# Kernel tuning notes

Measured on AMD Instinct MI355X. Metric: run time of the kernel, lower is better.

The kernel has to match this reference:

```python
import jax, jax.numpy as jnp
import numpy as np

K0 = 16                       # probe slice length (hard-coded in kernel)
TAU = 2.053748910631823       # t-test threshold (|tau| of kernel constant)


def setup_inputs() -> dict:
    key = jax.random.key(0)
    k1, k2, k3 = jax.random.split(key, 3)
    B, DIN, DOUT = 8192, 4096, 4096
    x = jax.random.normal(k1, (B, DIN), dtype=jnp.float32)
    W = jax.random.normal(k2, (DOUT, DIN), dtype=jnp.float32)
    bias = jax.random.normal(k3, (DOUT,), dtype=jnp.float32)
    return {"x": x, "W": W, "bias": bias}


def reference(x, W, bias):
    # --- partial dot over the first K0 columns of K (the probe) ---
    x0 = x[:, :K0]                    # [B, K0]
    w0 = W[:, :K0]                    # [DOUT, K0]
    y1 = x0 @ w0.T                    # [B, DOUT]  sum_k x_k * w_k
    # sum of squared elementwise products: prod_k^2 = x_k^2 * w_k^2
    s2 = (x0 * x0) @ (w0 * w0).T      # [B, DOUT]
    # --- per-(row, column) t-statistic and early-exit decision ---
    tstat = jnp.abs(y1) / jnp.sqrt(s2 / K0)
    passed = tstat < TAU              # True -> column deemed insignificant, zeroed
    # --- full linear (active columns keep full accumulation + bias) ---
    full = x @ W.T + bias[None, :]    # [B, DOUT]
    return jnp.where(passed, 0.0, full)
```

## Files before the change

kernel.cpp:

```cpp
#include <hip/hip_runtime.h>
#include <cstdint>
#include <cstddef>

#define TAU_D 2.053748910631823
#define M_DIM 8192
#define N_DIM 4096
#define K_DIM 4096
#define NT64  (K_DIM / 64)

typedef float f32x4 __attribute__((ext_vector_type(4)));
typedef short bf16x8 __attribute__((ext_vector_type(8)));

typedef __attribute__((address_space(1))) void gvoid_t;
typedef __attribute__((address_space(3))) void lvoid_t;

__device__ __forceinline__ void gload_lds16(const void* g, void* l) {
    __builtin_amdgcn_global_load_lds((const gvoid_t*)g, (lvoid_t*)l, 16, 0, 0);
}

__device__ __forceinline__ unsigned int pack2bf(float lo, float hi) {
    unsigned int ul = __float_as_uint(lo);
    unsigned int uh = __float_as_uint(hi);
    ul = (ul + 0x7FFFu + ((ul >> 16) & 1u)) >> 16;
    uh = (uh + 0x7FFFu + ((uh >> 16) & 1u)) >> 16;
    return ul | (uh << 16);
}

__global__ void cvt_f32_to_bf16(const float4* __restrict__ in,
                                uint2* __restrict__ out, int n4) {
    int i = blockIdx.x * blockDim.x + threadIdx.x;
    const int stride = gridDim.x * blockDim.x;
    for (; i < n4; i += stride) {
        float4 a = in[i];
        uint2 o;
        o.x = pack2bf(a.x, a.y);
        o.y = pack2bf(a.z, a.w);
        out[i] = o;
    }
}

__global__ __launch_bounds__(512, 2) void gemm_masked8(
    const unsigned short* __restrict__ Ab,
    const unsigned short* __restrict__ Bb,
    const float* __restrict__ X,
    const float* __restrict__ Wt,
    const float* __restrict__ bias,
    float* __restrict__ out)
{
    __shared__ __align__(16) char lds[131072];

    const int tid  = threadIdx.x;
    const int wave = tid >> 6;
    const int lane = tid & 63;
    const int lr = lane & 15;
    const int lq = lane >> 4;
    const int wm = wave >> 2;
    const int wn = wave & 3;

    const int flat = blockIdx.x;
    const int xcd  = flat & 7;
    const int s    = flat >> 3;
    const int rnd  = s >> 5;
    const int jj   = s & 31;
    const int trow = rnd * 16 + ((xcd >> 2) << 3) + (jj >> 2);
    const int tcol = ((xcd & 3) << 2) + (jj & 3);
    const int rowBase = trow * 256;
    const int colBase = tcol * 256;

    f32x4 acc[8][4];
    #pragma unroll
    for (int i = 0; i < 8; ++i)
        #pragma unroll
        for (int n = 0; n < 4; ++n)
            acc[i][n] = (f32x4){0.f, 0.f, 0.f, 0.f};

    const int srow  = tid >> 3;
    const int sslot = (tid & 7) ^ (srow & 7);
    const unsigned short* aSrc =
        Ab + (size_t)(rowBase + srow) * K_DIM + sslot * 8;
    const unsigned short* bSrc =
        Bb + (size_t)(colBase + srow) * K_DIM + sslot * 8;

    const unsigned baseA = (unsigned)(wm * 128 + lr) * 128;
    const unsigned baseB = 32768u + (unsigned)(wn * 64 + lr) * 128;
    const unsigned sk0 = (unsigned)((lq) ^ (lr & 7)) * 16;
    const unsigned sk1 = (unsigned)((4 + lq) ^ (lr & 7)) * 16;

    #pragma unroll
    for (int i = 0; i < 4; ++i)
        gload_lds16(aSrc + (size_t)i * 64 * K_DIM,
                    lds + i * 8192 + wave * 1024);
    #pragma unroll
    for (int i = 0; i < 4; ++i)
        gload_lds16(bSrc + (size_t)i * 64 * K_DIM,
                    lds + 32768 + i * 8192 + wave * 1024);
    __syncthreads();

    for (int T = 0; T < NT64; ++T) {
        const bool st = (T + 1 < NT64);
        const unsigned cb = (unsigned)(T & 1) << 16;
        const unsigned ob = cb ^ 65536u;
        const char* L = lds + cb;
        const unsigned short* aS = aSrc + (size_t)(T + 1) * 64;
        const unsigned short* bS = bSrc + (size_t)(T + 1) * 64;

        bf16x8 af[4], bq[4];

        #pragma unroll
        for (int m = 0; m < 4; ++m)
            af[m] = *(const bf16x8*)(L + baseA + m * 2048 + sk0);
        #pragma unroll
        for (int n = 0; n < 4; ++n)
            bq[n] = *(const bf16x8*)(L + baseB + n * 2048 + sk0);
        if (st) {
            #pragma unroll
            for (int i = 0; i < 4; ++i)
                gload_lds16(aS + (size_t)i * 64 * K_DIM,
                            lds + ob + i * 8192 + wave * 1024);
        }
        __builtin_amdgcn_s_barrier();
        __builtin_amdgcn_sched_barrier(0);
        __builtin_amdgcn_s_setprio(1);
        #pragma unroll
        for (int m = 0; m < 4; ++m)
            #pragma unroll
            for (int n = 0; n < 4; ++n)
                acc[m][n] = __builtin_amdgcn_mfma_f32_16x16x32_bf16(
                    af[m], bq[n], acc[m][n], 0, 0, 0);
        __builtin_amdgcn_s_setprio(0);
        __builtin_amdgcn_s_barrier();
        __builtin_amdgcn_sched_barrier(0);

        #pragma unroll
        for (int m = 0; m < 4; ++m)
            af[m] = *(const bf16x8*)(L + baseA + (4 + m) * 2048 + sk0);
        if (st) {
            #pragma unroll
            for (int i = 0; i < 4; ++i)
                gload_lds16(bS + (size_t)i * 64 * K_DIM,
                            lds + ob + 32768 + i * 8192 + wave * 1024);
        }
        __builtin_amdgcn_s_barrier();
        __builtin_amdgcn_sched_barrier(0);
        __builtin_amdgcn_s_setprio(1);
        #pragma unroll
        for (int m = 0; m < 4; ++m)
            #pragma unroll
            for (int n = 0; n < 4; ++n)
                acc[4 + m][n] = __builtin_amdgcn_mfma_f32_16x16x32_bf16(
                    af[m], bq[n], acc[4 + m][n], 0, 0, 0);
        __builtin_amdgcn_s_setprio(0);
        __builtin_amdgcn_s_barrier();
        __builtin_amdgcn_sched_barrier(0);

        #pragma unroll
        for (int m = 0; m < 4; ++m)
            af[m] = *(const bf16x8*)(L + baseA + m * 2048 + sk1);
        #pragma unroll
        for (int n = 0; n < 4; ++n)
            bq[n] = *(const bf16x8*)(L + baseB + n * 2048 + sk1);
        __builtin_amdgcn_s_barrier();
        __builtin_amdgcn_sched_barrier(0);
        __builtin_amdgcn_s_setprio(1);
        #pragma unroll
        for (int m = 0; m < 4; ++m)
            #pragma unroll
            for (int n = 0; n < 4; ++n)
                acc[m][n] = __builtin_amdgcn_mfma_f32_16x16x32_bf16(
                    af[m], bq[n], acc[m][n], 0, 0, 0);
        __builtin_amdgcn_s_setprio(0);
        __builtin_amdgcn_s_barrier();
        __builtin_amdgcn_sched_barrier(0);

        #pragma unroll
        for (int m = 0; m < 4; ++m)
            af[m] = *(const bf16x8*)(L + baseA + (4 + m) * 2048 + sk1);
        __builtin_amdgcn_s_barrier();
        __builtin_amdgcn_sched_barrier(0);
        __builtin_amdgcn_s_setprio(1);
        #pragma unroll
        for (int m = 0; m < 4; ++m)
            #pragma unroll
            for (int n = 0; n < 4; ++n)
                acc[4 + m][n] = __builtin_amdgcn_mfma_f32_16x16x32_bf16(
                    af[m], bq[n], acc[4 + m][n], 0, 0, 0);
        __builtin_amdgcn_s_setprio(0);

        __syncthreads();
    }

    float* x0s = (float*)(lds);
    float* w0s = (float*)(lds + 16384);
    #pragma unroll
    for (int i = 0; i < 2; ++i) {
        int idx = tid + i * 512;
        int r = idx >> 2, qq = (idx & 3) << 2;
        *(f32x4*)(x0s + r * 16 + qq) =
            *(const f32x4*)(X + (size_t)(rowBase + r) * K_DIM + qq);
        *(f32x4*)(w0s + r * 16 + qq) =
            *(const f32x4*)(Wt + (size_t)(colBase + r) * K_DIM + qq);
    }
    __syncthreads();

    const float TAU32 = (float)TAU_D;

    #pragma unroll
    for (int np = 0; np < 4; np += 2) {
        float wv[2][16];
        float bv[2];
        #pragma unroll
        for (int e = 0; e < 2; ++e) {
            const int c = wn * 64 + (np + e) * 16 + lr;
            #pragma unroll
            for (int q = 0; q < 4; ++q)
                *(f32x4*)&wv[e][q * 4] = *(const f32x4*)(w0s + c * 16 + q * 4);
            bv[e] = bias[colBase + c];
        }
        #pragma unroll
        for (int mi = 0; mi < 8; ++mi) {
            #pragma unroll
            for (int j = 0; j < 4; ++j) {
                const int rw = wm * 128 + mi * 16 + lq * 4 + j;
                float xv[16];
                #pragma unroll
                for (int q = 0; q < 4; ++q)
                    *(f32x4*)&xv[q * 4] = *(const f32x4*)(x0s + rw * 16 + q * 4);
                const size_t orow = (size_t)(rowBase + rw) * N_DIM + colBase;
                #pragma unroll
                for (int e = 0; e < 2; ++e) {
                    const int n = np + e;
                    float y1 = 0.f, s2 = 0.f;
                    #pragma unroll
                    for (int k = 0; k < 16; ++k) {
                        float xk = xv[k], wk = wv[e][k];
                        float xx = xk * xk, ww = wk * wk;
                        y1 = fmaf(xk, wk, y1);
                        s2 = fmaf(xx, ww, s2);
                    }
                    float t = fabsf(y1) / sqrtf(s2 * 0.0625f);
                    float v = (t < TAU32) ? 0.0f : (acc[mi][n][j] + bv[e]);
                    out[orow + wn * 64 + n * 16 + lr] = v;
                }
            }
        }
    }
}

__global__ __launch_bounds__(256, 2) void gemm_masked_fb(
    const float* __restrict__ X, const float* __restrict__ Wt,
    const float* __restrict__ bias, float* __restrict__ out)
{
    __shared__ __align__(16) unsigned short As[128 * 32];
    __shared__ __align__(16) unsigned short Bs[128 * 32];

    const int tid  = threadIdx.x;
    const int wave = tid >> 6;
    const int lane = tid & 63;
    const int rowBase = blockIdx.y * 128;
    const int colBase = blockIdx.x * 128;
    const int wr = wave >> 1;
    const int wc = wave & 1;
    const int lr = lane & 15;
    const int lq = lane >> 4;

    f32x4 acc[4][4];
    #pragma unroll
    for (int m = 0; m < 4; ++m)
        #pragma unroll
        for (int n = 0; n < 4; ++n)
            acc[m][n] = (f32x4){0.f, 0.f, 0.f, 0.f};

    const int srow = tid >> 2;
    const int scol = (tid & 3) * 8;
    const float* afp = X  + (size_t)(rowBase + srow) * K_DIM + scol;
    const float* bfp = Wt + (size_t)(colBase + srow) * K_DIM + scol;

    for (int kt = 0; kt < K_DIM; kt += 32) {
        #pragma unroll
        for (int issue = 0; issue < 2; ++issue) {
            const float* sa = afp + (size_t)issue * 64 * K_DIM;
            const float* sb = bfp + (size_t)issue * 64 * K_DIM;
            float4 a0 = *(const float4*)(sa);
            float4 a1 = *(const float4*)(sa + 4);
            float4 b0 = *(const float4*)(sb);
            float4 b1 = *(const float4*)(sb + 4);
            uint4 pa, pb;
            pa.x = pack2bf(a0.x, a0.y); pa.y = pack2bf(a0.z, a0.w);
            pa.z = pack2bf(a1.x, a1.y); pa.w = pack2bf(a1.z, a1.w);
            pb.x = pack2bf(b0.x, b0.y); pb.y = pack2bf(b0.z, b0.w);
            pb.z = pack2bf(b1.x, b1.y); pb.w = pack2bf(b1.z, b1.w);
            *(uint4*)((char*)As + issue * 4096 + tid * 16) = pa;
            *(uint4*)((char*)Bs + issue * 4096 + tid * 16) = pb;
        }
        afp += 32; bfp += 32;
        __syncthreads();

        bf16x8 af[4], bq[4];
        #pragma unroll
        for (int m = 0; m < 4; ++m)
            af[m] = *(const bf16x8*)(As + (wr * 64 + m * 16 + lr) * 32 + lq * 8);
        #pragma unroll
        for (int n = 0; n < 4; ++n)
            bq[n] = *(const bf16x8*)(Bs + (wc * 64 + n * 16 + lr) * 32 + lq * 8);
        #pragma unroll
        for (int m = 0; m < 4; ++m)
            #pragma unroll
            for (int n = 0; n < 4; ++n)
                acc[m][n] = __builtin_amdgcn_mfma_f32_16x16x32_bf16(
                    af[m], bq[n], acc[m][n], 0, 0, 0);
        __syncthreads();
    }

    float* x0s = (float*)As;
    float* w0s = (float*)Bs;
    #pragma unroll
    for (int i = 0; i < 2; ++i) {
        int idx = tid + i * 256;
        int r = idx >> 2, q = (idx & 3) * 4;
        *(float4*)(x0s + r * 16 + q) =
            *(const float4*)(X + (size_t)(rowBase + r) * K_DIM + q);
        *(float4*)(w0s + r * 16 + q) =
            *(const float4*)(Wt + (size_t)(colBase + r) * K_DIM + q);
    }
    __syncthreads();

    const float TAU32 = (float)TAU_D;
    float wv[4][16];
    float bv[4];
    #pragma unroll
    for (int n = 0; n < 4; ++n) {
        int c = wc * 64 + n * 16 + lr;
        #pragma unroll
        for (int q = 0; q < 4; ++q)
            *(f32x4*)&wv[n][q * 4] = *(const f32x4*)(w0s + c * 16 + q * 4);
        bv[n] = bias[colBase + c];
    }

    #pragma unroll
    for (int m = 0; m < 4; ++m) {
        #pragma unroll
        for (int j = 0; j < 4; ++j) {
            const int r = wr * 64 + m * 16 + lq * 4 + j;
            float xv[16];
            #pragma unroll
            for (int q = 0; q < 4; ++q)
                *(f32x4*)&xv[q * 4] = *(const f32x4*)(x0s + r * 16 + q * 4);
            const size_t orow = (size_t)(rowBase + r) * N_DIM + colBase;
            #pragma unroll
            for (int n = 0; n < 4; ++n) {
                float y1 = 0.f, s2 = 0.f;
                #pragma unroll
                for (int k = 0; k < 16; ++k) {
                    float xk = xv[k];
                    float wk = wv[n][k];
                    float xx = xk * xk;
                    float ww = wk * wk;
                    y1 = fmaf(xk, wk, y1);
                    s2 = fmaf(xx, ww, s2);
                }
                float t = fabsf(y1) / sqrtf(s2 * 0.0625f);
                float v = (t < TAU32) ? 0.0f : (acc[m][n][j] + bv[n]);
                out[orow + wc * 64 + n * 16 + lr] = v;
            }
        }
    }
}

extern "C" void kernel_launch(void* const* d_in, const int* in_sizes, int n_in,
                              void* d_out, int out_size, void* d_ws, size_t ws_size,
                              hipStream_t stream) {
    const float* x    = (const float*)d_in[0];
    const float* W    = (const float*)d_in[1];
    const float* bias = (const float*)d_in[2];
    float* out = (float*)d_out;

    const size_t needA = (size_t)M_DIM * K_DIM * 2;
    const size_t needB = (size_t)N_DIM * K_DIM * 2;

    if (ws_size >= needA + needB) {
        unsigned short* xb = (unsigned short*)d_ws;
        unsigned short* wb = (unsigned short*)((char*)d_ws + needA);
        cvt_f32_to_bf16<<<2048, 256, 0, stream>>>(
            (const float4*)x, (uint2*)xb, (M_DIM * K_DIM) / 4);
        cvt_f32_to_bf16<<<2048, 256, 0, stream>>>(
            (const float4*)W, (uint2*)wb, (N_DIM * K_DIM) / 4);
        dim3 grid((M_DIM / 256) * (N_DIM / 256));
        gemm_masked8<<<grid, 512, 0, stream>>>(xb, wb, x, W, bias, out);
    } else {
        dim3 grid(N_DIM / 128, M_DIM / 128);
        gemm_masked_fb<<<grid, 256, 0, stream>>>(x, W, bias, out);
    }
}
```

Baseline: 331.2 us.

## Switch GEMM main loop to triple-buffered K=32 stages with vmcnt-based waits

Measured after the change: 353.1 us. 1.07x slower.

```diff
diff --git a/kernel.cpp b/kernel.cpp
--- a/kernel.cpp
+++ b/kernel.cpp
@@ -6,7 +6,7 @@
 #define M_DIM 8192
 #define N_DIM 4096
 #define K_DIM 4096
-#define NT64  (K_DIM / 64)
+#define NT32  (K_DIM / 32)
 
 typedef float f32x4 __attribute__((ext_vector_type(4)));
 typedef short bf16x8 __attribute__((ext_vector_type(8)));
@@ -47,7 +47,7 @@
     const float* __restrict__ bias,
     float* __restrict__ out)
 {
-    __shared__ __align__(16) char lds[131072];
+    __shared__ __align__(16) char lds[98304];
 
     const int tid  = threadIdx.x;
     const int wave = tid >> 6;
@@ -74,49 +74,54 @@
         for (int n = 0; n < 4; ++n)
             acc[i][n] = (f32x4){0.f, 0.f, 0.f, 0.f};
 
-    const int srow  = tid >> 3;
-    const int sslot = (tid & 7) ^ (srow & 7);
+    const int srow = tid >> 2;
+    const int slog = ((tid & 3) - ((tid >> 3) & 3)) & 3;
     const unsigned short* aSrc =
-        Ab + (size_t)(rowBase + srow) * K_DIM + sslot * 8;
+        Ab + (size_t)(rowBase + srow) * K_DIM + slog * 8;
     const unsigned short* bSrc =
-        Bb + (size_t)(colBase + srow) * K_DIM + sslot * 8;
-
-    const unsigned baseA = (unsigned)(wm * 128 + lr) * 128;
-    const unsigned baseB = 32768u + (unsigned)(wn * 64 + lr) * 128;
-    const unsigned sk0 = (unsigned)((lq) ^ (lr & 7)) * 16;
-    const unsigned sk1 = (unsigned)((4 + lq) ^ (lr & 7)) * 16;
-
-    #pragma unroll
-    for (int i = 0; i < 4; ++i)
-        gload_lds16(aSrc + (size_t)i * 64 * K_DIM,
-                    lds + i * 8192 + wave * 1024);
-    #pragma unroll
-    for (int i = 0; i < 4; ++i)
-        gload_lds16(bSrc + (size_t)i * 64 * K_DIM,
-                    lds + 32768 + i * 8192 + wave * 1024);
-    __syncthreads();
-
-    for (int T = 0; T < NT64; ++T) {
-        const bool st = (T + 1 < NT64);
-        const unsigned cb = (unsigned)(T & 1) << 16;
-        const unsigned ob = cb ^ 65536u;
-        const char* L = lds + cb;
-        const unsigned short* aS = aSrc + (size_t)(T + 1) * 64;
-        const unsigned short* bS = bSrc + (size_t)(T + 1) * 64;
+        Bb + (size_t)(colBase + srow) * K_DIM + slog * 8;
+
+    const unsigned skrot = (unsigned)((lq + (lr >> 1)) & 3) * 16;
+    const unsigned offA0 = (unsigned)(wm * 128 + lr) * 64 + skrot;
+    const unsigned offB0 = 16384u + (unsigned)(wn * 64 + lr) * 64 + skrot;
+
+    unsigned b0 = 0, b1 = 32768, b2 = 65536;
+
+    #pragma unroll
+    for (int i = 0; i < 2; ++i)
+        gload_lds16(aSrc + (size_t)i * 128 * K_DIM, lds + b0 + i * 8192 + wave * 1024);
+    #pragma unroll
+    for (int i = 0; i < 2; ++i)
+        gload_lds16(bSrc + (size_t)i * 128 * K_DIM, lds + b0 + 16384 + i * 8192 + wave * 1024);
+    #pragma unroll
+    for (int i = 0; i < 2; ++i)
+        gload_lds16(aSrc + 32 + (size_t)i * 128 * K_DIM, lds + b1 + i * 8192 + wave * 1024);
+    #pragma unroll
+    for (int i = 0; i < 2; ++i)
+        gload_lds16(bSrc + 32 + (size_t)i * 128 * K_DIM, lds + b1 + 16384 + i * 8192 + wave * 1024);
+    asm volatile("s_waitcnt vmcnt(4)" ::: "memory");
+    __builtin_amdgcn_s_barrier();
+    __builtin_amdgcn_sched_barrier(0);
+
+    for (int T = 0; T < NT32; ++T) {
+        const bool st = (T + 2 < NT32);
+        const char* L = lds + b0;
+        const unsigned short* aS = aSrc + (size_t)(T + 2) * 32;
+        const unsigned short* bS = bSrc + (size_t)(T + 2) * 32;
 
         bf16x8 af[4], bq[4];
 
         #pragma unroll
         for (int m = 0; m < 4; ++m)
-            af[m] = *(const bf16x8*)(L + baseA + m * 2048 + sk0);
+            af[m] = *(const bf16x8*)(L + offA0 + m * 1024);
         #pragma unroll
         for (int n = 0; n < 4; ++n)
-            bq[n] = *(const bf16x8*)(L + baseB + n * 2048 + sk0);
+            bq[n] = *(const bf16x8*)(L + offB0 + n * 1024);
         if (st) {
             #pragma unroll
-            for (int i = 0; i < 4; ++i)
-                gload_lds16(aS + (size_t)i * 64 * K_DIM,
-                            lds + ob + i * 8192 + wave * 1024);
+            for (int i = 0; i < 2; ++i)
+                gload_lds16(aS + (size_t)i * 128 * K_DIM,
+                            lds + b2 + i * 8192 + wave * 1024);
         }
         __builtin_amdgcn_s_barrier();
         __builtin_amdgcn_sched_barrier(0);
@@ -133,12 +138,12 @@
 
         #pragma unroll
         for (int m = 0; m < 4; ++m)
-            af[m] = *(const bf16x8*)(L + baseA + (4 + m) * 2048 + sk0);
+            af[m] = *(const bf16x8*)(L + offA0 + (4 + m) * 1024);
         if (st) {
             #pragma unroll
-            for (int i = 0; i < 4; ++i)
-                gload_lds16(bS + (size_t)i * 64 * K_DIM,
-                            lds + ob + 32768 + i * 8192 + wave * 1024);
+            for (int i = 0; i < 2; ++i)
+                gload_lds16(bS + (size_t)i * 128 * K_DIM,
+                            lds + b2 + 16384 + i * 8192 + wave * 1024);
         }
         __builtin_amdgcn_s_barrier();
         __builtin_amdgcn_sched_barrier(0);
@@ -150,43 +155,16 @@
                 acc[4 + m][n] = __builtin_amdgcn_mfma_f32_16x16x32_bf16(
                     af[m], bq[n], acc[4 + m][n], 0, 0, 0);
         __builtin_amdgcn_s_setprio(0);
+
+        if (T < NT32 - 2) {
+            asm volatile("s_waitcnt vmcnt(4)" ::: "memory");
+        } else if (T == NT32 - 2) {
+            asm volatile("s_waitcnt vmcnt(0)" ::: "memory");
+        }
         __builtin_amdgcn_s_barrier();
         __builtin_amdgcn_sched_barrier(0);
 
-        #pragma unroll
-        for (int m = 0; m < 4; ++m)
-            af[m] = *(const bf16x8*)(L + baseA + m * 2048 + sk1);
-        #pragma unroll
-        for (int n = 0; n < 4; ++n)
-            bq[n] = *(const bf16x8*)(L + baseB + n * 2048 + sk1);
-        __builtin_amdgcn_s_barrier();
-        __builtin_amdgcn_sched_barrier(0);
-        __builtin_amdgcn_s_setprio(1);
-        #pragma unroll
-        for (int m = 0; m < 4; ++m)
-            #pragma unroll
-            for (int n = 0; n < 4; ++n)
-                acc[m][n] = __builtin_amdgcn_mfma_f32_16x16x32_bf16(
-                    af[m], bq[n], acc[m][n], 0, 0, 0);
-        __builtin_amdgcn_s_setprio(0);
-        __builtin_amdgcn_s_barrier();
-        __builtin_amdgcn_sched_barrier(0);
-
-        #pragma unroll
-        for (int m = 0; m < 4; ++m)
-            af[m] = *(const bf16x8*)(L + baseA + (4 + m) * 2048 + sk1);
-        __builtin_amdgcn_s_barrier();
-        __builtin_amdgcn_sched_barrier(0);
-        __builtin_amdgcn_s_setprio(1);
-        #pragma unroll
-        for (int m = 0; m < 4; ++m)
-            #pragma unroll
-            for (int n = 0; n < 4; ++n)
-                acc[4 + m][n] = __builtin_amdgcn_mfma_f32_16x16x32_bf16(
-                    af[m], bq[n], acc[4 + m][n], 0, 0, 0);
-        __builtin_amdgcn_s_setprio(0);
-
-        __syncthreads();
+        unsigned t = b0; b0 = b1; b1 = b2; b2 = t;
     }
 
     float* x0s = (float*)(lds);
```

## Restructure GEMM main loop into an 8-phase pipeline with split A/B LDS staging

Applied to the files above, without the earlier changes.

Measured after the change: 325.0 us. About the same (-1.9%).

```diff
diff --git a/kernel.cpp b/kernel.cpp
--- a/kernel.cpp
+++ b/kernel.cpp
@@ -6,9 +6,9 @@
 #define M_DIM 8192
 #define N_DIM 4096
 #define K_DIM 4096
-#define NT64  (K_DIM / 64)
-
-typedef float f32x4 __attribute__((ext_vector_type(4)));
+#define NIT   32
+
+typedef float f32x4  __attribute__((ext_vector_type(4)));
 typedef short bf16x8 __attribute__((ext_vector_type(8)));
 
 typedef __attribute__((address_space(1))) void gvoid_t;
@@ -39,6 +39,9 @@
     }
 }
 
+#define BARRIER() do { __builtin_amdgcn_s_barrier(); \
+                       __builtin_amdgcn_sched_barrier(0); } while (0)
+
 __global__ __launch_bounds__(512, 2) void gemm_masked8(
     const unsigned short* __restrict__ Ab,
     const unsigned short* __restrict__ Bb,
@@ -81,114 +84,197 @@
     const unsigned short* bSrc =
         Bb + (size_t)(colBase + srow) * K_DIM + sslot * 8;
 
-    const unsigned baseA = (unsigned)(wm * 128 + lr) * 128;
-    const unsigned baseB = 32768u + (unsigned)(wn * 64 + lr) * 128;
-    const unsigned sk0 = (unsigned)((lq) ^ (lr & 7)) * 16;
-    const unsigned sk1 = (unsigned)((4 + lq) ^ (lr & 7)) * 16;
-
-    #pragma unroll
-    for (int i = 0; i < 4; ++i)
-        gload_lds16(aSrc + (size_t)i * 64 * K_DIM,
-                    lds + i * 8192 + wave * 1024);
-    #pragma unroll
-    for (int i = 0; i < 4; ++i)
-        gload_lds16(bSrc + (size_t)i * 64 * K_DIM,
-                    lds + 32768 + i * 8192 + wave * 1024);
+    const unsigned R0A = 0, R0B = 32768, R1A = 65536, R1B = 98304;
+
+    auto stageA = [&](int kst, unsigned reg) {
+        #pragma unroll
+        for (int i = 0; i < 4; ++i)
+            gload_lds16(aSrc + (size_t)i * 64 * K_DIM + kst * 64,
+                        lds + reg + i * 8192 + wave * 1024);
+    };
+    auto stageB = [&](int kst, unsigned reg) {
+        #pragma unroll
+        for (int i = 0; i < 4; ++i)
+            gload_lds16(bSrc + (size_t)i * 64 * K_DIM + kst * 64,
+                        lds + reg + i * 8192 + wave * 1024);
+    };
+
+    const unsigned kk0 = (unsigned)((lq) ^ (lr & 7)) * 16;
+    const unsigned kk1 = (unsigned)((4 + lq) ^ (lr & 7)) * 16;
+    const unsigned rowA = (unsigned)(wm * 128 + lr) * 128;
+    const unsigned rowB = (unsigned)(wn * 64 + lr) * 128;
+
+    stageA(0, R0A);
+    stageB(0, R0B);
+    stageA(1, R1A);
+    asm volatile("s_waitcnt vmcnt(4)" ::: "memory");
+    BARRIER();
+
+    bf16x8 aF[4][2];
+    bf16x8 bF0[2][2];
+    bf16x8 bF1[2][2];
+
+    for (int j = 0; j < NIT; ++j) {
+        const int ka = 2 * j;
+        const int kb = 2 * j + 1;
+        const bool stg = (j + 1 < NIT);
+
+        #pragma unroll
+        for (int m = 0; m < 4; ++m) {
+            aF[m][0] = *(const bf16x8*)(lds + R0A + rowA + m * 2048 + kk0);
+            aF[m][1] = *(const bf16x8*)(lds + R0A + rowA + m * 2048 + kk1);
+        }
+        #pragma unroll
+        for (int n = 0; n < 2; ++n) {
+            bF0[n][0] = *(const bf16x8*)(lds + R0B + rowB + n * 2048 + kk0);
+            bF0[n][1] = *(const bf16x8*)(lds + R0B + rowB + n * 2048 + kk1);
+        }
+        stageB(kb, R1B);
+        BARRIER();
+        __builtin_amdgcn_s_setprio(1);
+        #pragma unroll
+        for (int m = 0; m < 4; ++m)
+            #pragma unroll
+            for (int n = 0; n < 2; ++n)
+                #pragma unroll
+                for (int ks = 0; ks < 2; ++ks)
+                    acc[m][n] = __builtin_amdgcn_mfma_f32_16x16x32_bf16(
+                        aF[m][ks], bF0[n][ks], acc[m][n], 0, 0, 0);
+        __builtin_amdgcn_s_setprio(0);
+        BARRIER();
+
+        #pragma unroll
+        for (int n = 0; n < 2; ++n) {
+            bF1[n][0] = *(const bf16x8*)(lds + R0B + rowB + (2 + n) * 2048 + kk0);
+            bF1[n][1] = *(const bf16x8*)(lds + R0B + rowB + (2 + n) * 2048 + kk1);
+        }
+        BARRIER();
+        __builtin_amdgcn_s_setprio(1);
+        #pragma unroll
+        for (int m = 0; m < 4; ++m)
+            #pragma unroll
+            for (int n = 0; n < 2; ++n)
+                #pragma unroll
+                for (int ks = 0; ks < 2; ++ks)
+                    acc[m][2 + n] = __builtin_amdgcn_mfma_f32_16x16x32_bf16(
+                        aF[m][ks], bF1[n][ks], acc[m][2 + n], 0, 0, 0);
+        __builtin_amdgcn_s_setprio(0);
+        BARRIER();
+
+        #pragma unroll
+        for (int m = 0; m < 4; ++m) {
+            aF[m][0] = *(const bf16x8*)(lds + R0A + rowA + (4 + m) * 2048 + kk0);
+            aF[m][1] = *(const bf16x8*)(lds + R0A + rowA + (4 + m) * 2048 + kk1);
+        }
+        BARRIER();
+        __builtin_amdgcn_s_setprio(1);
+        #pragma unroll
+        for (int m = 0; m < 4; ++m)
+            #pragma unroll
+            for (int n = 0; n < 2; ++n)
+                #pragma unroll
+                for (int ks = 0; ks < 2; ++ks)
+                    acc[4 + m][2 + n] = __builtin_amdgcn_mfma_f32_16x16x32_bf16(
+                        aF[m][ks], bF1[n][ks], acc[4 + m][2 + n], 0, 0, 0);
+        __builtin_amdgcn_s_setprio(0);
+        BARRIER();
+
+        if (stg) stageA(ka + 2, R0A);
+        BARRIER();
+        __builtin_amdgcn_s_setprio(1);
+        #pragma unroll
+        for (int m = 0; m < 4; ++m)
+            #pragma unroll
+            for (int n = 0; n < 2; ++n)
+                #pragma unroll
+                for (int ks = 0; ks < 2; ++ks)
+                    acc[4 + m][n] = __builtin_amdgcn_mfma_f32_16x16x32_bf16(
+                        aF[m][ks], bF0[n][ks], acc[4 + m][n], 0, 0, 0);
+        __builtin_amdgcn_s_setprio(0);
+        if (stg) {
+            asm volatile("s_waitcnt vmcnt(4)" ::: "memory");
+        } else {
+            asm volatile("s_waitcnt vmcnt(0)" ::: "memory");
+        }
+        BARRIER();
+
+        #pragma unroll
+        for (int m = 0; m < 4; ++m) {
+            aF[m][0] = *(const bf16x8*)(lds + R1A + rowA + m * 2048 + kk0);
+            aF[m][1] = *(const bf16x8*)(lds + R1A + rowA + m * 2048 + kk1);
+        }
+        #pragma unroll
+        for (int n = 0; n < 2; ++n) {
+            bF0[n][0] = *(const bf16x8*)(lds + R1B + rowB + n * 2048 + kk0);
+            bF0[n][1] = *(const bf16x8*)(lds + R1B + rowB + n * 2048 + kk1);
+        }
+        if (stg) stageB(ka + 2, R0B);
+        BARRIER();
+        __builtin_amdgcn_s_setprio(1);
+        #pragma unroll
+        for (int m = 0; m < 4; ++m)
+            #pragma unroll
+            for (int n = 0; n < 2; ++n)
+                #pragma unroll
+                for (int ks = 0; ks < 2; ++ks)
+                    acc[m][n] = __builtin_amdgcn_mfma_f32_16x16x32_bf16(
+                        aF[m][ks], bF0[n][ks], acc[m][n], 0, 0, 0);
+        __builtin_amdgcn_s_setprio(0);
+        BARRIER();
+
+        #pragma unroll
+        for (int n = 0; n < 2; ++n) {
+            bF1[n][0] = *(const bf16x8*)(lds + R1B + rowB + (2 + n) * 2048 + kk0);
+            bF1[n][1] = *(const bf16x8*)(lds + R1B + rowB + (2 + n) * 2048 + kk1);
+        }
+        BARRIER();
+        __builtin_amdgcn_s_setprio(1);
+        #pragma unroll
+        for (int m = 0; m < 4; ++m)
+            #pragma unroll
+            for (int n = 0; n < 2; ++n)
+                #pragma unroll
+                for (int ks = 0; ks < 2; ++ks)
+                    acc[m][2 + n] = __builtin_amdgcn_mfma_f32_16x16x32_bf16(
+                        aF[m][ks], bF1[n][ks], acc[m][2 + n], 0, 0, 0);
+        __builtin_amdgcn_s_setprio(0);
+        BARRIER();
+
+        #pragma unroll
+        for (int m = 0; m < 4; ++m) {
+            aF[m][0] = *(const bf16x8*)(lds + R1A + rowA + (4 + m) * 2048 + kk0);
+            aF[m][1] = *(const bf16x8*)(lds + R1A + rowA + (4 + m) * 2048 + kk1);
+        }
+        BARRIER();
+        __builtin_amdgcn_s_setprio(1);
+        #pragma unroll
+        for (int m = 0; m < 4; ++m)
+            #pragma unroll
+            for (int n = 0; n < 2; ++n)
+                #pragma unroll
+                for (int ks = 0; ks < 2; ++ks)
+                    acc[4 + m][2 + n] = __builtin_amdgcn_mfma_f32_16x16x32_bf16(
+                        aF[m][ks], bF1[n][ks], acc[4 + m][2 + n], 0, 0, 0);
+        __builtin_amdgcn_s_setprio(0);
+        BARRIER();
+
+        if (stg) stageA(kb + 2, R1A);
+        BARRIER();
+        __builtin_amdgcn_s_setprio(1);
+        #pragma unroll
+        for (int m = 0; m < 4; ++m)
+            #pragma unroll
+            for (int n = 0; n < 2; ++n)
+                #pragma unroll
+                for (int ks = 0; ks < 2; ++ks)
+                    acc[4 + m][n] = __builtin_amdgcn_mfma_f32_16x16x32_bf16(
+                        aF[m][ks], bF0[n][ks], acc[4 + m][n], 0, 0, 0);
+        __builtin_amdgcn_s_setprio(0);
+        asm volatile("s_waitcnt vmcnt(4)" ::: "memory");
+        BARRIER();
+    }
+
     __syncthreads();
-
-    for (int T = 0; T < NT64; ++T) {
-        const bool st = (T + 1 < NT64);
-        const unsigned cb = (unsigned)(T & 1) << 16;
-        const unsigned ob = cb ^ 65536u;
-        const char* L = lds + cb;
-        const unsigned short* aS = aSrc + (size_t)(T + 1) * 64;
-        const unsigned short* bS = bSrc + (size_t)(T + 1) * 64;
-
-        bf16x8 af[4], bq[4];
-
-        #pragma unroll
-        for (int m = 0; m < 4; ++m)
-            af[m] = *(const bf16x8*)(L + baseA + m * 2048 + sk0);
-        #pragma unroll
-        for (int n = 0; n < 4; ++n)
-            bq[n] = *(const bf16x8*)(L + baseB + n * 2048 + sk0);
-        if (st) {
-            #pragma unroll
-            for (int i = 0; i < 4; ++i)
-                gload_lds16(aS + (size_t)i * 64 * K_DIM,
-                            lds + ob + i * 8192 + wave * 1024);
-        }
-        __builtin_amdgcn_s_barrier();
-        __builtin_amdgcn_sched_barrier(0);
-        __builtin_amdgcn_s_setprio(1);
-        #pragma unroll
-        for (int m = 0; m < 4; ++m)
-            #pragma unroll
-            for (int n = 0; n < 4; ++n)
-                acc[m][n] = __builtin_amdgcn_mfma_f32_16x16x32_bf16(
-                    af[m], bq[n], acc[m][n], 0, 0, 0);
-        __builtin_amdgcn_s_setprio(0);
-        __builtin_amdgcn_s_barrier();
-        __builtin_amdgcn_sched_barrier(0);
-
-        #pragma unroll
-        for (int m = 0; m < 4; ++m)
-            af[m] = *(const bf16x8*)(L + baseA + (4 + m) * 2048 + sk0);
-        if (st) {
-            #pragma unroll
-            for (int i = 0; i < 4; ++i)
-                gload_lds16(bS + (size_t)i * 64 * K_DIM,
-                            lds + ob + 32768 + i * 8192 + wave * 1024);
-        }
-        __builtin_amdgcn_s_barrier();
-        __builtin_amdgcn_sched_barrier(0);
-        __builtin_amdgcn_s_setprio(1);
-        #pragma unroll
-        for (int m = 0; m < 4; ++m)
-            #pragma unroll
-            for (int n = 0; n < 4; ++n)
-                acc[4 + m][n] = __builtin_amdgcn_mfma_f32_16x16x32_bf16(
-                    af[m], bq[n], acc[4 + m][n], 0, 0, 0);
-        __builtin_amdgcn_s_setprio(0);
-        __builtin_amdgcn_s_barrier();
-        __builtin_amdgcn_sched_barrier(0);
-
-        #pragma unroll
-        for (int m = 0; m < 4; ++m)
-            af[m] = *(const bf16x8*)(L + baseA + m * 2048 + sk1);
-        #pragma unroll
-        for (int n = 0; n < 4; ++n)
-            bq[n] = *(const bf16x8*)(L + baseB + n * 2048 + sk1);
-        __builtin_amdgcn_s_barrier();
-        __builtin_amdgcn_sched_barrier(0);
-        __builtin_amdgcn_s_setprio(1);
-        #pragma unroll
-        for (int m = 0; m < 4; ++m)
-            #pragma unroll
-            for (int n = 0; n < 4; ++n)
-                acc[m][n] = __builtin_amdgcn_mfma_f32_16x16x32_bf16(
-                    af[m], bq[n], acc[m][n], 0, 0, 0);
-        __builtin_amdgcn_s_setprio(0);
-        __builtin_amdgcn_s_barrier();
-        __builtin_amdgcn_sched_barrier(0);
-
-        #pragma unroll
-        for (int m = 0; m < 4; ++m)
-            af[m] = *(const bf16x8*)(L + baseA + (4 + m) * 2048 + sk1);
-        __builtin_amdgcn_s_barrier();
-        __builtin_amdgcn_sched_barrier(0);
-        __builtin_amdgcn_s_setprio(1);
-        #pragma unroll
-        for (int m = 0; m < 4; ++m)
-            #pragma unroll
-            for (int n = 0; n < 4; ++n)
-                acc[4 + m][n] = __builtin_amdgcn_mfma_f32_16x16x32_bf16(
-                    af[m], bq[n], acc[4 + m][n], 0, 0, 0);
-        __builtin_amdgcn_s_setprio(0);
-
-        __syncthreads();
-    }
-
     float* x0s = (float*)(lds);
     float* w0s = (float*)(lds + 16384);
     #pragma unroll
@@ -219,8 +305,8 @@
         #pragma unroll
         for (int mi = 0; mi < 8; ++mi) {
             #pragma unroll
-            for (int j = 0; j < 4; ++j) {
-                const int rw = wm * 128 + mi * 16 + lq * 4 + j;
+            for (int jr = 0; jr < 4; ++jr) {
+                const int rw = wm * 128 + mi * 16 + lq * 4 + jr;
                 float xv[16];
                 #pragma unroll
                 for (int q = 0; q < 4; ++q)
@@ -238,7 +324,7 @@
                         s2 = fmaf(xx, ww, s2);
                     }
                     float t = fabsf(y1) / sqrtf(s2 * 0.0625f);
-                    float v = (t < TAU32) ? 0.0f : (acc[mi][n][j] + bv[e]);
+                    float v = (t < TAU32) ? 0.0f : (acc[mi][n][jr] + bv[e]);
                     out[orow + wn * 64 + n * 16 + lr] = v;
                 }
             }
```
